# Kernel tuning notes

Hardware: AMD Instinct MI355X
Metric: run time of the kernel (lower is better)

Reference implementation:

```python
import jax, jax.numpy as jnp
import numpy as np


def setup_inputs() -> dict:
    key = jax.random.key(0)
    k1, k2, k3 = jax.random.split(key, 3)
    B, S, D_IN, D_OUT, R = 4, 2048, 4096, 4096, 8
    x = jax.random.normal(k1, (B, S, D_IN), dtype=jnp.float32)
    # fixed_linear.weight: [out_features, in_features]
    weight = jax.random.normal(k2, (D_OUT, D_IN), dtype=jnp.float32) * 0.02
    # hra_u: [in_features, r] Householder vectors
    hra_u = jax.random.normal(k3, (D_IN, R), dtype=jnp.float32)
    return {"x": x, "weight": weight, "hra_u": hra_u}


def reference(x, weight, hra_u):
    # Normalize each Householder vector (column) as in the torch module.
    u = hra_u / jnp.linalg.norm(hra_u, axis=0, keepdims=True)  # [in, r]

    # Sequentially apply W <- W (I - 2 u u^T) == W - 2 (W u) u^T  (rank-1 update,
    # mathematically identical to the original's explicit [in,in] GEMM per step).
    def step(w, ui):  # w: [out, in], ui: [in]
        wu = w @ ui                      # [out]
        return w - 2.0 * jnp.outer(wu, ui), None

    new_weight, _ = jax.lax.scan(step, weight, u.T)  # scan over r reflections

    # F.linear(x, new_weight) = x @ new_weight^T, bias=False
    return jnp.einsum("bsd,od->bso", x, new_weight)
```

## Files before the change

kernel.cpp:

```cpp
#include <hip/hip_runtime.h>
#include <hip/hip_bf16.h>


#define D_IN   4096
#define D_OUT  4096
#define R_HH   8
#define M_ROWS 8192

typedef short bf16x8  __attribute__((ext_vector_type(8)));
typedef float f32x4   __attribute__((ext_vector_type(4)));
typedef float f32x16  __attribute__((ext_vector_type(16)));

__device__ inline unsigned short f2bf(float f) {
    unsigned int x = __float_as_uint(f);
    unsigned int lsb = (x >> 16) & 1u;
    x += 0x7fffu + lsb;
    return (unsigned short)(x >> 16);
}

__device__ inline void async16(const unsigned short* g, char* l) {
    __builtin_amdgcn_global_load_lds(
        (const __attribute__((address_space(1))) void*)g,
        (__attribute__((address_space(3))) void*)l,
        16, 0, 0);
}

__global__ __launch_bounds__(1024) void prep(const float* __restrict__ hu,
                                             float* __restrict__ G,
                                             float* __restrict__ inv8) {
    float d[36];
    #pragma unroll
    for (int p = 0; p < 36; p++) d[p] = 0.f;
    for (int r = threadIdx.x; r < D_IN; r += 1024) {
        const float4* h4 = (const float4*)&hu[r * R_HH];
        float4 a = h4[0], b = h4[1];
        float h[8] = {a.x, a.y, a.z, a.w, b.x, b.y, b.z, b.w};
        int p = 0;
        #pragma unroll
        for (int i = 0; i < 8; i++)
            #pragma unroll
            for (int j = i; j < 8; j++)
                d[p++] += h[i] * h[j];
    }
    #pragma unroll
    for (int p = 0; p < 36; p++)
        #pragma unroll
        for (int off = 32; off > 0; off >>= 1)
            d[p] += __shfl_down(d[p], off, 64);
    __shared__ float red[16 * 36];
    const int wave = threadIdx.x >> 6, lane = threadIdx.x & 63;
    if (lane == 0)
        #pragma unroll
        for (int p = 0; p < 36; p++) red[wave * 36 + p] = d[p];
    __syncthreads();
    __shared__ float dd[36];
    if (threadIdx.x < 36) {
        float s = 0.f;
        #pragma unroll
        for (int w = 0; w < 16; w++) s += red[w * 36 + threadIdx.x];
        dd[threadIdx.x] = s;
    }
    __syncthreads();
    auto idx = [](int a, int b) { return a * 8 + b - (a * (a + 1)) / 2; };
    if (threadIdx.x < 64) {
        const int i = threadIdx.x >> 3, j = threadIdx.x & 7;
        const int a = i < j ? i : j, b = i < j ? j : i;
        const float gi = rsqrtf(dd[idx(i, i)]);
        const float gj = rsqrtf(dd[idx(j, j)]);
        G[threadIdx.x] = dd[idx(a, b)] * gi * gj;
        if (j == 0) inv8[i] = gi;
    }
}

__global__ void wu_gemv(const float* __restrict__ W, const float* __restrict__ hu,
                        const float* __restrict__ inv8, float* __restrict__ Y) {
    const int o = blockIdx.x;
    const float* wrow = W + (size_t)o * D_IN;
    float acc[8] = {0,0,0,0,0,0,0,0};
    for (int k = threadIdx.x; k < D_IN; k += 256) {
        float w = wrow[k];
        const float4* u4 = (const float4*)&hu[k * R_HH];
        float4 a = u4[0], b = u4[1];
        acc[0] += w * a.x; acc[1] += w * a.y; acc[2] += w * a.z; acc[3] += w * a.w;
        acc[4] += w * b.x; acc[5] += w * b.y; acc[6] += w * b.z; acc[7] += w * b.w;
    }
    __shared__ float red[8 * 256];
    #pragma unroll
    for (int j = 0; j < 8; j++) red[j * 256 + threadIdx.x] = acc[j];
    __syncthreads();
    for (int off = 128; off > 0; off >>= 1) {
        if (threadIdx.x < off)
            #pragma unroll
            for (int j = 0; j < 8; j++)
                red[j * 256 + threadIdx.x] += red[j * 256 + threadIdx.x + off];
        __syncthreads();
    }
    if (threadIdx.x < 8)
        Y[(size_t)o * R_HH + threadIdx.x] = red[threadIdx.x * 256] * inv8[threadIdx.x];
}

__global__ void wn_cast(const float* __restrict__ W, const float* __restrict__ hu,
                        const float* __restrict__ inv8, const float* __restrict__ Y,
                        const float* __restrict__ G, unsigned short* __restrict__ Wn) {
    const int o = blockIdx.x;
    __shared__ float gs[64];
    __shared__ float ys[8];
    __shared__ float is[8];
    if (threadIdx.x < 64) gs[threadIdx.x] = G[threadIdx.x];
    else if (threadIdx.x < 72) ys[threadIdx.x - 64] = Y[(size_t)o * R_HH + threadIdx.x - 64];
    else if (threadIdx.x < 80) is[threadIdx.x - 72] = inv8[threadIdx.x - 72];
    __syncthreads();
    float v[8];
    #pragma unroll
    for (int i = 0; i < 8; i++) {
        float t = ys[i];
        #pragma unroll
        for (int j = 0; j < 8; j++)
            if (j < i) t -= 2.0f * gs[j * 8 + i] * v[j];
        v[i] = t;
    }
    #pragma unroll
    for (int i = 0; i < 8; i++) v[i] *= is[i];
    const float4* wrow = (const float4*)(W + (size_t)o * D_IN);
    ushort4* wnrow = (ushort4*)(Wn + (size_t)o * D_IN);
    for (int k4 = threadIdx.x; k4 < D_IN / 4; k4 += 256) {
        float4 wv = wrow[k4];
        float wa[4] = {wv.x, wv.y, wv.z, wv.w};
        float out[4];
        #pragma unroll
        for (int e = 0; e < 4; e++) {
            const int k = k4 * 4 + e;
            const float4* u4 = (const float4*)&hu[k * R_HH];
            float4 ua = u4[0], ub = u4[1];
            float corr = v[0]*ua.x + v[1]*ua.y + v[2]*ua.z + v[3]*ua.w
                       + v[4]*ub.x + v[5]*ub.y + v[6]*ub.z + v[7]*ub.w;
            out[e] = wa[e] - 2.0f * corr;
        }
        ushort4 r;
        r.x = f2bf(out[0]); r.y = f2bf(out[1]); r.z = f2bf(out[2]); r.w = f2bf(out[3]);
        wnrow[k4] = r;
    }
}

__global__ void cast_x(const float4* __restrict__ x, ushort4* __restrict__ xb, int n4) {
    for (int g = blockIdx.x * 256 + threadIdx.x; g < n4; g += gridDim.x * 256) {
        float4 f = x[g];
        ushort4 r;
        r.x = f2bf(f.x); r.y = f2bf(f.y); r.z = f2bf(f.z); r.w = f2bf(f.w);
        xb[g] = r;
    }
}

__global__ __launch_bounds__(512, 2) void gemm256(
    const unsigned short* __restrict__ A,
    const unsigned short* __restrict__ B,
    float* __restrict__ C) {
    constexpr int K  = D_IN;
    constexpr int NN = D_OUT;
    constexpr int NT = K / 64;

    extern __shared__ __align__(16) char lds[];

    const int tid  = threadIdx.x;
    const int lane = tid & 63;
    const int wave = tid >> 6;

    const int bid = blockIdx.x;
    const int cpx = gridDim.x >> 3;
    const int swz = (bid & 7) * cpx + (bid >> 3);
    const int TN  = NN / 256;
    const int tm  = swz / TN, tn = swz - tm * TN;

    const size_t rA0 = (size_t)tm * 256;
    const size_t rB0 = (size_t)tn * 256;

    const int wr = (wave >> 2) * 128;
    const int wc = (wave & 3) * 64;

    const int sRow = tid >> 2;
    const int sCol = ((tid & 3) * 8) ^ ((sRow & 8) ? 16 : 0);
    const unsigned short* gA = A + (rA0 + sRow) * (size_t)K + sCol;
    const unsigned short* gB = B + (rB0 + sRow) * (size_t)K + sCol;

    auto stageA = [&](int kt, int h) {
        const unsigned short* g = gA + (size_t)(h * 128) * K + kt * 64;
        char* l = lds + (kt & 1) * 32768 + h * 8192 + tid * 16;
        async16(g, l);
        async16(g + 32, l + 16384);
    };
    auto stageB = [&](int kt, int h) {
        const unsigned short* g = gB + (size_t)(h * 128) * K + kt * 64;
        char* l = lds + 65536 + (kt & 1) * 32768 + h * 8192 + tid * 16;
        async16(g, l);
        async16(g + 32, l + 16384);
    };

    const int xorv = (lane & 8) ? 32 : 0;
    const int k16  = (lane >> 5) * 16;
    const int rbA  = (wr + (lane & 31)) * 64;
    const int rbB  = (wc + (lane & 31)) * 64;

    auto LDA = [&](int bb, int i, int s) -> bf16x8 {
        return *(const bf16x8*)(lds + bb * 32768 + (s >> 1) * 16384
                                + i * 2048 + rbA + (((s & 1) * 32 + k16) ^ xorv));
    };
    auto LDB = [&](int bb, int j, int s) -> bf16x8 {
        return *(const bf16x8*)(lds + 65536 + bb * 32768 + (s >> 1) * 16384
                                + j * 2048 + rbB + (((s & 1) * 32 + k16) ^ xorv));
    };

    f32x16 acc[4][2];
    #pragma unroll
    for (int i = 0; i < 4; i++)
        #pragma unroll
        for (int j = 0; j < 2; j++)
            acc[i][j] = (f32x16){0.f,0.f,0.f,0.f,0.f,0.f,0.f,0.f,
                                 0.f,0.f,0.f,0.f,0.f,0.f,0.f,0.f};

    stageA(0, 0); stageA(0, 1); stageB(0, 0); stageB(0, 1);
    stageB(1, 0); stageB(1, 1);
    asm volatile("s_waitcnt vmcnt(4)" ::: "memory");
    __builtin_amdgcn_s_barrier();

    #pragma unroll 2
    for (int kt = 0; kt < NT; ++kt) {
        const int bb = kt & 1;

        bf16x8 a[2][4], b[2][4];
        #pragma unroll
        for (int i = 0; i < 2; i++)
            #pragma unroll
            for (int s = 0; s < 4; s++) a[i][s] = LDA(bb, i, s);
        #pragma unroll
        for (int j = 0; j < 2; j++)
            #pragma unroll
            for (int s = 0; s < 4; s++) b[j][s] = LDB(bb, j, s);
        if (kt + 1 < NT) stageA(kt + 1, 0);
        __builtin_amdgcn_s_setprio(1);
        #pragma unroll
        for (int s = 0; s < 2; s++)
            #pragma unroll
            for (int i = 0; i < 2; i++)
                #pragma unroll
                for (int j = 0; j < 2; j++)
                    acc[i][j] = __builtin_amdgcn_mfma_f32_32x32x16_bf16(a[i][s], b[j][s], acc[i][j], 0, 0, 0);
        __builtin_amdgcn_s_setprio(0);
        if (kt + 1 < NT) stageA(kt + 1, 1);
        __builtin_amdgcn_s_setprio(1);
        #pragma unroll
        for (int s = 2; s < 4; s++)
            #pragma unroll
            for (int i = 0; i < 2; i++)
                #pragma unroll
                for (int j = 0; j < 2; j++)
                    acc[i][j] = __builtin_amdgcn_mfma_f32_32x32x16_bf16(a[i][s], b[j][s], acc[i][j], 0, 0, 0);
        __builtin_amdgcn_s_setprio(0);

        asm volatile("" ::: "memory");
        __builtin_amdgcn_s_barrier();
        asm volatile("" ::: "memory");

        #pragma unroll
        for (int i = 0; i < 2; i++)
            #pragma unroll
            for (int s = 0; s < 4; s++) a[i][s] = LDA(bb, 2 + i, s);
        if (kt + 2 < NT) stageB(kt + 2, 0);
        __builtin_amdgcn_s_setprio(1);
        #pragma unroll
        for (int s = 0; s < 2; s++)
            #pragma unroll
            for (int i = 0; i < 2; i++)
                #pragma unroll
                for (int j = 0; j < 2; j++)
                    acc[2 + i][j] = __builtin_amdgcn_mfma_f32_32x32x16_bf16(a[i][s], b[j][s], acc[2 + i][j], 0, 0, 0);
        __builtin_amdgcn_s_setprio(0);
        if (kt + 2 < NT) stageB(kt + 2, 1);
        __builtin_amdgcn_s_setprio(1);
        #pragma unroll
        for (int s = 2; s < 4; s++)
            #pragma unroll
            for (int i = 0; i < 2; i++)
                #pragma unroll
                for (int j = 0; j < 2; j++)
                    acc[2 + i][j] = __builtin_amdgcn_mfma_f32_32x32x16_bf16(a[i][s], b[j][s], acc[2 + i][j], 0, 0, 0);
        __builtin_amdgcn_s_setprio(0);

        if (kt < NT - 2)
            asm volatile("s_waitcnt vmcnt(4)" ::: "memory");
        else
            asm volatile("s_waitcnt vmcnt(0)" ::: "memory");
        __builtin_amdgcn_s_barrier();
    }

    const int ccol = lane & 31;
    const int rsub = 4 * (lane >> 5);
    #pragma unroll
    for (int i = 0; i < 4; i++) {
        #pragma unroll
        for (int j = 0; j < 2; j++) {
            size_t base = (rA0 + wr + i * 32 + rsub) * (size_t)NN
                        + (rB0 + wc + j * 32 + ccol);
            #pragma unroll
            for (int r = 0; r < 16; r++) {
                const int row = (r & 3) + 8 * (r >> 2);
                C[base + (size_t)row * NN] = acc[i][j][r];
            }
        }
    }
}

extern "C" void kernel_launch(void* const* d_in, const int* in_sizes, int n_in,
                              void* d_out, int out_size, void* d_ws, size_t ws_size,
                              hipStream_t stream) {
    const float* x      = (const float*)d_in[0];
    const float* weight = (const float*)d_in[1];
    const float* hra_u  = (const float*)d_in[2];
    float* out = (float*)d_out;

    char* w = (char*)d_ws;
    unsigned short* Xb = (unsigned short*)w;
    unsigned short* Wn = (unsigned short*)(w + (size_t)64 * 1024 * 1024);
    float* Y   = (float*)(w + (size_t)96 * 1024 * 1024);
    float* G   = Y + (size_t)D_IN * R_HH;
    float* inv = G + 64;

    static int attr_done = 0;
    if (!attr_done) {
        hipFuncSetAttribute((const void*)gemm256,
                            hipFuncAttributeMaxDynamicSharedMemorySize, 131072);
        attr_done = 1;
    }

    prep<<<1, 1024, 0, stream>>>(hra_u, G, inv);
    wu_gemv<<<D_OUT, 256, 0, stream>>>(weight, hra_u, inv, Y);
    wn_cast<<<D_OUT, 256, 0, stream>>>(weight, hra_u, inv, Y, G, Wn);

    const int n4 = M_ROWS * D_IN / 4;
    cast_x<<<4096, 256, 0, stream>>>((const float4*)x, (ushort4*)Xb, n4);

    gemm256<<<dim3((M_ROWS / 256) * (D_OUT / 256)), 512, 131072, stream>>>(Xb, Wn, out);
}
```

Baseline: 612.3 us.

## Fuse W·u GEMV with weight update and relayout GEMM LDS staging

Merges the two per-row weight kernels into one that keeps the fp32 weight row in registers, so W is read from HBM once instead of twice and the Y buffer round trip disappears. The GEMM's LDS staging is also changed from a row-major tile with an XOR swizzle to a k-chunk-major layout where each 16-byte k-slice of all 256 rows is stored contiguously. The new layout simplifies LDS addressing but drops the bank-conflict swizzle, so read conflicts may change.

```diff
diff --git a/kernel.cpp b/kernel.cpp
--- a/kernel.cpp
+++ b/kernel.cpp
@@ -72,60 +72,64 @@
     }
 }
 
-__global__ void wu_gemv(const float* __restrict__ W, const float* __restrict__ hu,
-                        const float* __restrict__ inv8, float* __restrict__ Y) {
+__global__ __launch_bounds__(256) void wuwn(
+    const float* __restrict__ W, const float* __restrict__ hu,
+    const float* __restrict__ inv8, const float* __restrict__ G,
+    unsigned short* __restrict__ Wn) {
     const int o = blockIdx.x;
-    const float* wrow = W + (size_t)o * D_IN;
+    const int t = threadIdx.x;
+    __shared__ float gs[64];
+    __shared__ float is[8];
+    if (t < 64) gs[t] = G[t];
+    if (t >= 64 && t < 72) is[t - 64] = inv8[t - 64];
+
+    const float4* wrow4 = (const float4*)(W + (size_t)o * D_IN);
+    float4 wreg[4];
     float acc[8] = {0,0,0,0,0,0,0,0};
-    for (int k = threadIdx.x; k < D_IN; k += 256) {
-        float w = wrow[k];
-        const float4* u4 = (const float4*)&hu[k * R_HH];
-        float4 a = u4[0], b = u4[1];
-        acc[0] += w * a.x; acc[1] += w * a.y; acc[2] += w * a.z; acc[3] += w * a.w;
-        acc[4] += w * b.x; acc[5] += w * b.y; acc[6] += w * b.z; acc[7] += w * b.w;
+    #pragma unroll
+    for (int c = 0; c < 4; c++) {
+        const int k4 = t + c * 256;
+        wreg[c] = wrow4[k4];
+        float wa[4] = {wreg[c].x, wreg[c].y, wreg[c].z, wreg[c].w};
+        #pragma unroll
+        for (int e = 0; e < 4; e++) {
+            const int k = k4 * 4 + e;
+            const float4* u4 = (const float4*)&hu[k * R_HH];
+            float4 ua = u4[0], ub = u4[1];
+            acc[0] += wa[e]*ua.x; acc[1] += wa[e]*ua.y;
+            acc[2] += wa[e]*ua.z; acc[3] += wa[e]*ua.w;
+            acc[4] += wa[e]*ub.x; acc[5] += wa[e]*ub.y;
+            acc[6] += wa[e]*ub.z; acc[7] += wa[e]*ub.w;
+        }
     }
     __shared__ float red[8 * 256];
     #pragma unroll
-    for (int j = 0; j < 8; j++) red[j * 256 + threadIdx.x] = acc[j];
+    for (int j = 0; j < 8; j++) red[j * 256 + t] = acc[j];
     __syncthreads();
     for (int off = 128; off > 0; off >>= 1) {
-        if (threadIdx.x < off)
+        if (t < off)
             #pragma unroll
             for (int j = 0; j < 8; j++)
-                red[j * 256 + threadIdx.x] += red[j * 256 + threadIdx.x + off];
+                red[j * 256 + t] += red[j * 256 + t + off];
         __syncthreads();
     }
-    if (threadIdx.x < 8)
-        Y[(size_t)o * R_HH + threadIdx.x] = red[threadIdx.x * 256] * inv8[threadIdx.x];
-}
-
-__global__ void wn_cast(const float* __restrict__ W, const float* __restrict__ hu,
-                        const float* __restrict__ inv8, const float* __restrict__ Y,
-                        const float* __restrict__ G, unsigned short* __restrict__ Wn) {
-    const int o = blockIdx.x;
-    __shared__ float gs[64];
-    __shared__ float ys[8];
-    __shared__ float is[8];
-    if (threadIdx.x < 64) gs[threadIdx.x] = G[threadIdx.x];
-    else if (threadIdx.x < 72) ys[threadIdx.x - 64] = Y[(size_t)o * R_HH + threadIdx.x - 64];
-    else if (threadIdx.x < 80) is[threadIdx.x - 72] = inv8[threadIdx.x - 72];
-    __syncthreads();
     float v[8];
     #pragma unroll
     for (int i = 0; i < 8; i++) {
-        float t = ys[i];
+        float ti = red[i * 256] * is[i];
         #pragma unroll
         for (int j = 0; j < 8; j++)
-            if (j < i) t -= 2.0f * gs[j * 8 + i] * v[j];
-        v[i] = t;
+            if (j < i) ti -= 2.0f * gs[j * 8 + i] * v[j];
+        v[i] = ti;
     }
     #pragma unroll
     for (int i = 0; i < 8; i++) v[i] *= is[i];
-    const float4* wrow = (const float4*)(W + (size_t)o * D_IN);
+
     ushort4* wnrow = (ushort4*)(Wn + (size_t)o * D_IN);
-    for (int k4 = threadIdx.x; k4 < D_IN / 4; k4 += 256) {
-        float4 wv = wrow[k4];
-        float wa[4] = {wv.x, wv.y, wv.z, wv.w};
+    #pragma unroll
+    for (int c = 0; c < 4; c++) {
+        const int k4 = t + c * 256;
+        float wa[4] = {wreg[c].x, wreg[c].y, wreg[c].z, wreg[c].w};
         float out[4];
         #pragma unroll
         for (int e = 0; e < 4; e++) {
@@ -177,36 +181,32 @@
     const int wr = (wave >> 2) * 128;
     const int wc = (wave & 3) * 64;
 
-    const int sRow = tid >> 2;
-    const int sCol = ((tid & 3) * 8) ^ ((sRow & 8) ? 16 : 0);
-    const unsigned short* gA = A + (rA0 + sRow) * (size_t)K + sCol;
-    const unsigned short* gB = B + (rB0 + sRow) * (size_t)K + sCol;
+    const int sRow2 = tid & 255;
+    const int sHi   = tid >> 8;
+    const unsigned short* gA2 = A + (rA0 + sRow2) * (size_t)K + sHi * 8;
+    const unsigned short* gB2 = B + (rB0 + sRow2) * (size_t)K + sHi * 8;
 
     auto stageA = [&](int kt, int h) {
-        const unsigned short* g = gA + (size_t)(h * 128) * K + kt * 64;
-        char* l = lds + (kt & 1) * 32768 + h * 8192 + tid * 16;
+        const unsigned short* g = gA2 + kt * 64 + h * 32;
+        char* l = lds + (kt & 1) * 32768 + h * 16384 + tid * 16;
         async16(g, l);
-        async16(g + 32, l + 16384);
+        async16(g + 16, l + 8192);
     };
     auto stageB = [&](int kt, int h) {
-        const unsigned short* g = gB + (size_t)(h * 128) * K + kt * 64;
-        char* l = lds + 65536 + (kt & 1) * 32768 + h * 8192 + tid * 16;
+        const unsigned short* g = gB2 + kt * 64 + h * 32;
+        char* l = lds + 65536 + (kt & 1) * 32768 + h * 16384 + tid * 16;
         async16(g, l);
-        async16(g + 32, l + 16384);
+        async16(g + 16, l + 8192);
     };
 
-    const int xorv = (lane & 8) ? 32 : 0;
-    const int k16  = (lane >> 5) * 16;
-    const int rbA  = (wr + (lane & 31)) * 64;
-    const int rbB  = (wc + (lane & 31)) * 64;
+    const int kAoff = (lane >> 5) * 4096 + (wr + (lane & 31)) * 16;
+    const int kBoff = 65536 + (lane >> 5) * 4096 + (wc + (lane & 31)) * 16;
 
     auto LDA = [&](int bb, int i, int s) -> bf16x8 {
-        return *(const bf16x8*)(lds + bb * 32768 + (s >> 1) * 16384
-                                + i * 2048 + rbA + (((s & 1) * 32 + k16) ^ xorv));
+        return *(const bf16x8*)(lds + bb * 32768 + s * 8192 + i * 512 + kAoff);
     };
     auto LDB = [&](int bb, int j, int s) -> bf16x8 {
-        return *(const bf16x8*)(lds + 65536 + bb * 32768 + (s >> 1) * 16384
-                                + j * 2048 + rbB + (((s & 1) * 32 + k16) ^ xorv));
+        return *(const bf16x8*)(lds + bb * 32768 + s * 8192 + j * 512 + kBoff);
     };
 
     f32x16 acc[4][2];
@@ -320,8 +320,7 @@
     char* w = (char*)d_ws;
     unsigned short* Xb = (unsigned short*)w;
     unsigned short* Wn = (unsigned short*)(w + (size_t)64 * 1024 * 1024);
-    float* Y   = (float*)(w + (size_t)96 * 1024 * 1024);
-    float* G   = Y + (size_t)D_IN * R_HH;
+    float* G   = (float*)(w + (size_t)96 * 1024 * 1024);
     float* inv = G + 64;
 
     static int attr_done = 0;
@@ -332,8 +331,7 @@
     }
 
     prep<<<1, 1024, 0, stream>>>(hra_u, G, inv);
-    wu_gemv<<<D_OUT, 256, 0, stream>>>(weight, hra_u, inv, Y);
-    wn_cast<<<D_OUT, 256, 0, stream>>>(weight, hra_u, inv, Y, G, Wn);
+    wuwn<<<D_OUT, 256, 0, stream>>>(weight, hra_u, inv, G, Wn);
 
     const int n4 = M_ROWS * D_IN / 4;
     cast_x<<<4096, 256, 0, stream>>>((const float4*)x, (ushort4*)Xb, n4);
```

Result: slower. 718.1 us (+17.3%).
